# Performance work log

Hardware: AMD Instinct MI355X
Metric: run time of the kernel (lower is better)

## Reference

```python
import jax, jax.numpy as jnp
import numpy as np

ACT_GUARD = 2.0   # 2 ** act_guard_bit (act_guard_bit = 1)
WGT_GUARD = 2.0   # 2 ** weight_guard_bit (weight_guard_bit = 1)


def _ste_round(v):
    # straight-through estimator round (QNMethod.STE)
    return v + jax.lax.stop_gradient(jnp.round(v) - v)


def setup_inputs() -> dict:
    key = jax.random.key(0)
    k_x, k_w, k_b = jax.random.split(key, 3)
    B, S, DIN, DOUT = 4, 2048, 2048, 8192
    ACT_INIT_S, ACT_INIT_Q, LOG_S_INIT = -10.0, 10.0, -8.0
    x = jax.random.normal(k_x, (B, S, DIN), dtype=jnp.float32)
    weight = jax.random.normal(k_w, (DOUT, DIN), dtype=jnp.float32) * 0.02
    bias = jax.random.normal(k_b, (DOUT,), dtype=jnp.float32) * 0.01
    log_act_s = jnp.full((1,), ACT_INIT_S, dtype=jnp.float32)
    log_act_q = jnp.full((1,), ACT_INIT_Q, dtype=jnp.float32)
    act_b = jnp.full((1,), -jnp.exp2(ACT_INIT_Q - 1.0), dtype=jnp.float32)  # -512
    log_wght_s = jnp.full((DOUT, 1), LOG_S_INIT, dtype=jnp.float32)
    return {"x": x, "weight": weight, "bias": bias, "log_act_s": log_act_s,
            "log_act_q": log_act_q, "act_b": act_b, "log_wght_s": log_wght_s}


def reference(x, weight, bias, log_act_s, log_act_q, act_b, log_wght_s):
    # --- activation fake-quant (per-tensor) ---
    s = jnp.exp2(log_act_s)                       # [1]
    q = jnp.exp2(log_act_q)                       # [1]
    zp = jnp.round(act_b / s * ACT_GUARD) / ACT_GUARD * s  # guard-bit rounded zero point
    lo, hi = zp, zp + q - s
    qx = _ste_round((jnp.clip(x, lo, hi) - zp) / s)
    x_dq = qx * s + zp                            # dequantized activations

    # --- weight fake-quant (per-channel over out dim, amin/amax over dim 1) ---
    w_scale = jnp.exp2(log_wght_s)                # [DOUT, 1]
    wmin = jnp.min(weight, axis=1, keepdims=True)
    wmax = jnp.max(weight, axis=1, keepdims=True)
    qwmin = jnp.round(wmin / w_scale * WGT_GUARD) / WGT_GUARD * w_scale
    qwmax = jnp.round(wmax / w_scale * WGT_GUARD) / WGT_GUARD * w_scale
    qw = _ste_round((jnp.clip(weight, qwmin, qwmax) - qwmin) / w_scale)
    w_dq = qw * w_scale + qwmin                   # dequantized weights

    # --- affine: y = x @ W.T + b ---
    return jnp.einsum('bsi,oi->bso', x_dq, w_dq) + bias
```

## Files before the change

### kernel.cpp

```cpp
#include <hip/hip_runtime.h>
#include <hip/hip_bf16.h>


using f16x8 = __attribute__((ext_vector_type(8))) _Float16;
using f32x4 = __attribute__((ext_vector_type(4))) float;

#define AS1 __attribute__((address_space(1)))
#define AS3 __attribute__((address_space(3)))

static __device__ __forceinline__ void gload_lds16(const void* g, void* l) {
    __builtin_amdgcn_global_load_lds((const AS1 void*)g, (AS3 void*)l, 16, 0, 0);
}

__global__ __launch_bounds__(256) void wquant_kernel(
    const float* __restrict__ W, const float* __restrict__ lws,
    _Float16* __restrict__ Wq) {
    constexpr int K = 2048;
    const int row = blockIdx.x;
    const int t = threadIdx.x;
    const float* w = W + (size_t)row * K;

    float4 v0 = ((const float4*)w)[t * 2];
    float4 v1 = ((const float4*)w)[t * 2 + 1];
    float vals[8] = {v0.x, v0.y, v0.z, v0.w, v1.x, v1.y, v1.z, v1.w};

    float mn = vals[0], mx = vals[0];
#pragma unroll
    for (int i = 1; i < 8; ++i) {
        mn = fminf(mn, vals[i]);
        mx = fmaxf(mx, vals[i]);
    }
#pragma unroll
    for (int off = 32; off >= 1; off >>= 1) {
        mn = fminf(mn, __shfl_xor(mn, off));
        mx = fmaxf(mx, __shfl_xor(mx, off));
    }
    __shared__ float smn[4], smx[4];
    if ((t & 63) == 0) { smn[t >> 6] = mn; smx[t >> 6] = mx; }
    __syncthreads();
    mn = fminf(fminf(smn[0], smn[1]), fminf(smn[2], smn[3]));
    mx = fmaxf(fmaxf(smx[0], smx[1]), fmaxf(smx[2], smx[3]));

    const float l = lws[row];
    const float ws = exp2f(l);
    const float rs = exp2f(-l);
    const float qwmin = rintf(mn * rs * 2.0f) * 0.5f * ws;
    const float qwmax = rintf(mx * rs * 2.0f) * 0.5f * ws;

    f16x8 out;
#pragma unroll
    for (int i = 0; i < 8; ++i) {
        float c = fminf(fmaxf(vals[i], qwmin), qwmax);
        float qw = rintf((c - qwmin) * rs);
        out[i] = (_Float16)(qw * ws + qwmin);
    }
    *(f16x8*)&Wq[(size_t)row * K + (size_t)t * 8] = out;
}

__global__ __launch_bounds__(256) void xquant_kernel(
    const float* __restrict__ X,
    const float* __restrict__ las, const float* __restrict__ laq,
    const float* __restrict__ ab, _Float16* __restrict__ Xq) {
    const float ls = las[0], lq = laq[0];
    const float s = exp2f(ls);
    const float rs = exp2f(-ls);
    const float q = exp2f(lq);
    const float zp = rintf(ab[0] * rs * 2.0f) * 0.5f * s;
    const float lo = zp;
    const float hi = (zp + q) - s;

    const size_t base = ((size_t)blockIdx.x * 256 + threadIdx.x) * 8;
    float4 v0 = *(const float4*)&X[base];
    float4 v1 = *(const float4*)&X[base + 4];
    float vals[8] = {v0.x, v0.y, v0.z, v0.w, v1.x, v1.y, v1.z, v1.w};

    f16x8 out;
#pragma unroll
    for (int i = 0; i < 8; ++i) {
        float c = fminf(fmaxf(vals[i], lo), hi);
        float qx = rintf((c - zp) * rs);
        out[i] = (_Float16)(qx * s + zp);
    }
    *(f16x8*)&Xq[base] = out;
}

__global__ __launch_bounds__(512, 2) void gemm_kernel(
    const _Float16* __restrict__ A, const _Float16* __restrict__ B,
    const float* __restrict__ bias, float* __restrict__ C) {
    constexpr int N = 8192, K = 2048;
    constexpr int KT = K / 64;
    constexpr int NBN = N / 256;

    __shared__ char smem[131072];
    char* As = smem;
    char* Bs = smem + 65536;

    const int bid = blockIdx.x;
    const int cpx = gridDim.x >> 3;
    const int swzb = (bid & 7) * cpx + (bid >> 3);
    const int bm = swzb / NBN;
    const int bn = swzb % NBN;

    const int t = threadIdx.x;
    const int lane = t & 63;
    const int wid = t >> 6;
    const int wr = wid >> 2;
    const int wc = wid & 3;
    const int l15 = lane & 15;
    const int lq = lane >> 4;

    const int c0 = t, c1 = t + 512;
    const int d0 = c0 * 16, d1 = c1 * 16;
    const int eoff0 = (d0 >> 6) * K + (((d0 & 63) ^ (((d0 >> 9) & 1) << 5)) >> 1);
    const int eoff1 = (d1 >> 6) * K + (((d1 & 63) ^ (((d1 >> 9) & 1) << 5)) >> 1);
    const _Float16* Agb = A + (size_t)bm * 256 * K;
    const _Float16* Bgb = B + (size_t)bn * 256 * K;

    const int colpart = (lq * 16) ^ ((l15 & 8) << 2);

    f32x4 acc[8][4] = {};

#define STAGE(gb, lm, ktSlot, ktSrc, ks) do {                                  \
        const _Float16* _g = (gb) + ((size_t)(ktSrc) * 64 + (ks) * 32);        \
        char* _l = (lm) + ((((ktSlot) & 1) * 2 + (ks)) * 16384);               \
        gload_lds16(_g + eoff0, _l + d0);                                      \
        gload_lds16(_g + eoff1, _l + d1);                                      \
    } while (0)

    STAGE(Bgb, Bs, 0, 0, 0);
    STAGE(Agb, As, 0, 0, 0);
    STAGE(Bgb, Bs, 0, 0, 1);
    STAGE(Agb, As, 0, 0, 1);
    STAGE(Bgb, Bs, 1, 1, 0);
    STAGE(Agb, As, 1, 1, 0);
    STAGE(Bgb, Bs, 1, 1, 1);
    asm volatile("s_waitcnt vmcnt(6)" ::: "memory");
    __builtin_amdgcn_s_barrier();

    for (int kt = 0; kt < KT; ++kt) {
        const int db = (kt & 1) * 2;
        const int s1 = kt + 1, s2 = kt + 2;
        const int s1c = (s1 < KT) ? s1 : (KT - 1);
        const int s2c = (s2 < KT) ? s2 : (KT - 1);

        f16x8 bf[4], af[4];

        {
            const char* Bsl = Bs + (db + 0) * 16384;
            const char* Asl = As + (db + 0) * 16384;
#pragma unroll
            for (int n = 0; n < 4; ++n)
                bf[n] = *(const f16x8*)(Bsl + (wc * 64 + n * 16 + l15) * 64 + colpart);
#pragma unroll
            for (int m = 0; m < 4; ++m)
                af[m] = *(const f16x8*)(Asl + (wr * 128 + m * 16 + l15) * 64 + colpart);
            STAGE(Agb, As, s1, s1c, 1);
            __builtin_amdgcn_s_barrier();
            asm volatile("s_waitcnt lgkmcnt(0)" ::: "memory");
            __builtin_amdgcn_sched_barrier(0);
            __builtin_amdgcn_s_setprio(1);
#pragma unroll
            for (int m = 0; m < 4; ++m)
#pragma unroll
                for (int n = 0; n < 4; ++n)
                    acc[m][n] = __builtin_amdgcn_mfma_f32_16x16x32_f16(
                        af[m], bf[n], acc[m][n], 0, 0, 0);
            __builtin_amdgcn_s_setprio(0);
            __builtin_amdgcn_s_barrier();
        }
        {
            const char* Asl = As + (db + 0) * 16384;
#pragma unroll
            for (int m = 0; m < 4; ++m)
                af[m] = *(const f16x8*)(Asl + (wr * 128 + 64 + m * 16 + l15) * 64 + colpart);
            STAGE(Bgb, Bs, s2, s2c, 0);
            __builtin_amdgcn_s_barrier();
            asm volatile("s_waitcnt lgkmcnt(0)" ::: "memory");
            __builtin_amdgcn_sched_barrier(0);
            __builtin_amdgcn_s_setprio(1);
#pragma unroll
            for (int m = 0; m < 4; ++m)
#pragma unroll
                for (int n = 0; n < 4; ++n)
                    acc[4 + m][n] = __builtin_amdgcn_mfma_f32_16x16x32_f16(
                        af[m], bf[n], acc[4 + m][n], 0, 0, 0);
            __builtin_amdgcn_s_setprio(0);
            __builtin_amdgcn_s_barrier();
        }
        {
            const char* Bsl = Bs + (db + 1) * 16384;
            const char* Asl = As + (db + 1) * 16384;
#pragma unroll
            for (int n = 0; n < 4; ++n)
                bf[n] = *(const f16x8*)(Bsl + (wc * 64 + n * 16 + l15) * 64 + colpart);
#pragma unroll
            for (int m = 0; m < 4; ++m)
                af[m] = *(const f16x8*)(Asl + (wr * 128 + m * 16 + l15) * 64 + colpart);
            STAGE(Agb, As, s2, s2c, 0);
            __builtin_amdgcn_s_barrier();
            asm volatile("s_waitcnt lgkmcnt(0)" ::: "memory");
            __builtin_amdgcn_sched_barrier(0);
            __builtin_amdgcn_s_setprio(1);
#pragma unroll
            for (int m = 0; m < 4; ++m)
#pragma unroll
                for (int n = 0; n < 4; ++n)
                    acc[m][n] = __builtin_amdgcn_mfma_f32_16x16x32_f16(
                        af[m], bf[n], acc[m][n], 0, 0, 0);
            __builtin_amdgcn_s_setprio(0);
            __builtin_amdgcn_s_barrier();
        }
        {
            const char* Asl = As + (db + 1) * 16384;
#pragma unroll
            for (int m = 0; m < 4; ++m)
                af[m] = *(const f16x8*)(Asl + (wr * 128 + 64 + m * 16 + l15) * 64 + colpart);
            STAGE(Bgb, Bs, s2, s2c, 1);
            __builtin_amdgcn_s_barrier();
            asm volatile("s_waitcnt lgkmcnt(0)" ::: "memory");
            __builtin_amdgcn_sched_barrier(0);
            __builtin_amdgcn_s_setprio(1);
#pragma unroll
            for (int m = 0; m < 4; ++m)
#pragma unroll
                for (int n = 0; n < 4; ++n)
                    acc[4 + m][n] = __builtin_amdgcn_mfma_f32_16x16x32_f16(
                        af[m], bf[n], acc[4 + m][n], 0, 0, 0);
            __builtin_amdgcn_s_setprio(0);
            asm volatile("s_waitcnt vmcnt(6)" ::: "memory");
            __builtin_amdgcn_s_barrier();
        }
    }
#undef STAGE

#pragma unroll
    for (int m = 0; m < 8; ++m) {
        const int row = bm * 256 + wr * 128 + m * 16 + lq * 4;
#pragma unroll
        for (int n = 0; n < 4; ++n) {
            const int col = bn * 256 + wc * 64 + n * 16 + l15;
            const float bv = bias[col];
#pragma unroll
            for (int r = 0; r < 4; ++r) {
                C[(size_t)(row + r) * N + col] = acc[m][n][r] + bv;
            }
        }
    }
}

extern "C" void kernel_launch(void* const* d_in, const int* in_sizes, int n_in,
                              void* d_out, int out_size, void* d_ws, size_t ws_size,
                              hipStream_t stream) {
    const float* x    = (const float*)d_in[0];
    const float* w    = (const float*)d_in[1];
    const float* bias = (const float*)d_in[2];
    const float* las  = (const float*)d_in[3];
    const float* laq  = (const float*)d_in[4];
    const float* ab   = (const float*)d_in[5];
    const float* lws  = (const float*)d_in[6];
    float* out = (float*)d_out;

    constexpr size_t MK = (size_t)8192 * 2048;
    _Float16* xq = (_Float16*)d_ws;
    _Float16* wq = (_Float16*)((char*)d_ws + MK * sizeof(_Float16));

    xquant_kernel<<<8192, 256, 0, stream>>>(x, las, laq, ab, xq);
    wquant_kernel<<<8192, 256, 0, stream>>>(w, lws, wq);
    gemm_kernel<<<1024, 512, 0, stream>>>(xq, wq, bias, out);
}
```

Baseline: 334.6 us.

## Software-pipeline LDS fragment loads with double-buffered registers across MFMA phases

```diff
diff --git a/kernel.cpp b/kernel.cpp
--- a/kernel.cpp
+++ b/kernel.cpp
@@ -109,8 +109,7 @@
     const int l15 = lane & 15;
     const int lq = lane >> 4;
 
-    const int c0 = t, c1 = t + 512;
-    const int d0 = c0 * 16, d1 = c1 * 16;
+    const int d0 = t * 16, d1 = (t + 512) * 16;
     const int eoff0 = (d0 >> 6) * K + (((d0 & 63) ^ (((d0 >> 9) & 1) << 5)) >> 1);
     const int eoff1 = (d1 >> 6) * K + (((d1 & 63) ^ (((d1 >> 9) & 1) << 5)) >> 1);
     const _Float16* Agb = A + (size_t)bm * 256 * K;
@@ -119,12 +118,38 @@
     const int colpart = (lq * 16) ^ ((l15 & 8) << 2);
 
     f32x4 acc[8][4] = {};
+    f16x8 afA[4], afB[4], bf0[4], bf1[4];
 
 #define STAGE(gb, lm, ktSlot, ktSrc, ks) do {                                  \
         const _Float16* _g = (gb) + ((size_t)(ktSrc) * 64 + (ks) * 32);        \
         char* _l = (lm) + ((((ktSlot) & 1) * 2 + (ks)) * 16384);               \
         gload_lds16(_g + eoff0, _l + d0);                                      \
         gload_lds16(_g + eoff1, _l + d1);                                      \
+    } while (0)
+
+#define LDA(dst, par, ks, mh) do {                                             \
+        const char* _s = As + ((par) * 2 + (ks)) * 16384;                      \
+        _Pragma("unroll")                                                      \
+        for (int _m = 0; _m < 4; ++_m)                                         \
+            dst[_m] = *(const f16x8*)(_s +                                     \
+                (wr * 128 + (mh) * 64 + _m * 16 + l15) * 64 + colpart);        \
+    } while (0)
+
+#define LDB(dst, par, ks) do {                                                 \
+        const char* _s = Bs + ((par) * 2 + (ks)) * 16384;                      \
+        _Pragma("unroll")                                                      \
+        for (int _n = 0; _n < 4; ++_n)                                         \
+            dst[_n] = *(const f16x8*)(_s +                                     \
+                (wc * 64 + _n * 16 + l15) * 64 + colpart);                     \
+    } while (0)
+
+#define MFMA16(accRow, afv, bfv) do {                                          \
+        _Pragma("unroll")                                                      \
+        for (int _m = 0; _m < 4; ++_m)                                         \
+            _Pragma("unroll")                                                  \
+            for (int _n = 0; _n < 4; ++_n)                                     \
+                acc[(accRow) + _m][_n] = __builtin_amdgcn_mfma_f32_16x16x32_f16(\
+                    afv[_m], bfv[_n], acc[(accRow) + _m][_n], 0, 0, 0);        \
     } while (0)
 
     STAGE(Bgb, Bs, 0, 0, 0);
@@ -136,102 +161,51 @@
     STAGE(Bgb, Bs, 1, 1, 1);
     asm volatile("s_waitcnt vmcnt(6)" ::: "memory");
     __builtin_amdgcn_s_barrier();
+    LDA(afA, 0, 0, 0);
+    LDB(bf0, 0, 0);
 
     for (int kt = 0; kt < KT; ++kt) {
-        const int db = (kt & 1) * 2;
-        const int s1 = kt + 1, s2 = kt + 2;
-        const int s1c = (s1 < KT) ? s1 : (KT - 1);
-        const int s2c = (s2 < KT) ? s2 : (KT - 1);
-
-        f16x8 bf[4], af[4];
-
-        {
-            const char* Bsl = Bs + (db + 0) * 16384;
-            const char* Asl = As + (db + 0) * 16384;
-#pragma unroll
-            for (int n = 0; n < 4; ++n)
-                bf[n] = *(const f16x8*)(Bsl + (wc * 64 + n * 16 + l15) * 64 + colpart);
-#pragma unroll
-            for (int m = 0; m < 4; ++m)
-                af[m] = *(const f16x8*)(Asl + (wr * 128 + m * 16 + l15) * 64 + colpart);
-            STAGE(Agb, As, s1, s1c, 1);
-            __builtin_amdgcn_s_barrier();
-            asm volatile("s_waitcnt lgkmcnt(0)" ::: "memory");
-            __builtin_amdgcn_sched_barrier(0);
-            __builtin_amdgcn_s_setprio(1);
-#pragma unroll
-            for (int m = 0; m < 4; ++m)
-#pragma unroll
-                for (int n = 0; n < 4; ++n)
-                    acc[m][n] = __builtin_amdgcn_mfma_f32_16x16x32_f16(
-                        af[m], bf[n], acc[m][n], 0, 0, 0);
-            __builtin_amdgcn_s_setprio(0);
-            __builtin_amdgcn_s_barrier();
-        }
-        {
-            const char* Asl = As + (db + 0) * 16384;
-#pragma unroll
-            for (int m = 0; m < 4; ++m)
-                af[m] = *(const f16x8*)(Asl + (wr * 128 + 64 + m * 16 + l15) * 64 + colpart);
-            STAGE(Bgb, Bs, s2, s2c, 0);
-            __builtin_amdgcn_s_barrier();
-            asm volatile("s_waitcnt lgkmcnt(0)" ::: "memory");
-            __builtin_amdgcn_sched_barrier(0);
-            __builtin_amdgcn_s_setprio(1);
-#pragma unroll
-            for (int m = 0; m < 4; ++m)
-#pragma unroll
-                for (int n = 0; n < 4; ++n)
-                    acc[4 + m][n] = __builtin_amdgcn_mfma_f32_16x16x32_f16(
-                        af[m], bf[n], acc[4 + m][n], 0, 0, 0);
-            __builtin_amdgcn_s_setprio(0);
-            __builtin_amdgcn_s_barrier();
-        }
-        {
-            const char* Bsl = Bs + (db + 1) * 16384;
-            const char* Asl = As + (db + 1) * 16384;
-#pragma unroll
-            for (int n = 0; n < 4; ++n)
-                bf[n] = *(const f16x8*)(Bsl + (wc * 64 + n * 16 + l15) * 64 + colpart);
-#pragma unroll
-            for (int m = 0; m < 4; ++m)
-                af[m] = *(const f16x8*)(Asl + (wr * 128 + m * 16 + l15) * 64 + colpart);
-            STAGE(Agb, As, s2, s2c, 0);
-            __builtin_amdgcn_s_barrier();
-            asm volatile("s_waitcnt lgkmcnt(0)" ::: "memory");
-            __builtin_amdgcn_sched_barrier(0);
-            __builtin_amdgcn_s_setprio(1);
-#pragma unroll
-            for (int m = 0; m < 4; ++m)
-#pragma unroll
-                for (int n = 0; n < 4; ++n)
-                    acc[m][n] = __builtin_amdgcn_mfma_f32_16x16x32_f16(
-                        af[m], bf[n], acc[m][n], 0, 0, 0);
-            __builtin_amdgcn_s_setprio(0);
-            __builtin_amdgcn_s_barrier();
-        }
-        {
-            const char* Asl = As + (db + 1) * 16384;
-#pragma unroll
-            for (int m = 0; m < 4; ++m)
-                af[m] = *(const f16x8*)(Asl + (wr * 128 + 64 + m * 16 + l15) * 64 + colpart);
-            STAGE(Bgb, Bs, s2, s2c, 1);
-            __builtin_amdgcn_s_barrier();
-            asm volatile("s_waitcnt lgkmcnt(0)" ::: "memory");
-            __builtin_amdgcn_sched_barrier(0);
-            __builtin_amdgcn_s_setprio(1);
-#pragma unroll
-            for (int m = 0; m < 4; ++m)
-#pragma unroll
-                for (int n = 0; n < 4; ++n)
-                    acc[4 + m][n] = __builtin_amdgcn_mfma_f32_16x16x32_f16(
-                        af[m], bf[n], acc[4 + m][n], 0, 0, 0);
-            __builtin_amdgcn_s_setprio(0);
-            asm volatile("s_waitcnt vmcnt(6)" ::: "memory");
-            __builtin_amdgcn_s_barrier();
-        }
+        const int par = kt & 1;
+        const int npar = par ^ 1;
+        const int nx = (kt + 1 < KT) ? kt + 1 : KT - 1;
+        const int s2 = (kt + 2 < KT) ? kt + 2 : KT - 1;
+
+        LDA(afB, par, 0, 1);
+        STAGE(Agb, As, kt + 1, nx, 1);
+        __builtin_amdgcn_s_setprio(1);
+        MFMA16(0, afA, bf0);
+        __builtin_amdgcn_s_setprio(0);
+        asm volatile("s_waitcnt vmcnt(8)" ::: "memory");
+        __builtin_amdgcn_s_barrier();
+
+        LDA(afA, par, 1, 0);
+        LDB(bf1, par, 1);
+        STAGE(Bgb, Bs, kt + 2, s2, 0);
+        __builtin_amdgcn_s_setprio(1);
+        MFMA16(4, afB, bf0);
+        __builtin_amdgcn_s_setprio(0);
+        __builtin_amdgcn_s_barrier();
+
+        LDA(afB, par, 1, 1);
+        STAGE(Agb, As, kt + 2, s2, 0);
+        __builtin_amdgcn_s_setprio(1);
+        MFMA16(0, afA, bf1);
+        __builtin_amdgcn_s_setprio(0);
+        asm volatile("s_waitcnt vmcnt(8)" ::: "memory");
+        __builtin_amdgcn_s_barrier();
+
+        LDA(afA, npar, 0, 0);
+        LDB(bf0, npar, 0);
+        STAGE(Bgb, Bs, kt + 2, s2, 1);
+        __builtin_amdgcn_s_setprio(1);
+        MFMA16(4, afB, bf1);
+        __builtin_amdgcn_s_setprio(0);
+        __builtin_amdgcn_s_barrier();
     }
 #undef STAGE
+#undef LDA
+#undef LDB
+#undef MFMA16
 
 #pragma unroll
     for (int m = 0; m < 8; ++m) {
```

After: 331.3 us. No clear change (-1.0%).
